# Performance work log

Measured on AMD Instinct MI355X. Metric: run time of the kernel, lower is better.

## Reference

```python
import jax, jax.numpy as jnp
import numpy as np

DIM = 1024
NUM_HEADS = 16
HEAD_DIM = DIM // NUM_HEADS


def setup_inputs() -> dict:
    key = jax.random.key(0)
    k1, k2, k3, k4, k5 = jax.random.split(key, 5)
    s = 0.02
    return {
        "x": jax.random.normal(k1, (2, 2048, DIM), dtype=jnp.float32),
        "Wq": jax.random.normal(k2, (DIM, DIM), dtype=jnp.float32) * s,
        "Wk": jax.random.normal(k3, (DIM, DIM), dtype=jnp.float32) * s,
        "Wv": jax.random.normal(k4, (DIM, DIM), dtype=jnp.float32) * s,
        "Wo": jax.random.normal(k5, (DIM, DIM), dtype=jnp.float32) * s,
    }


def rotate_half(x):
    x1, x2 = x[..., : x.shape[-1] // 2], x[..., x.shape[-1] // 2 :]
    return jnp.concatenate([-x2, x1], axis=-1)


def rope_cos_sin(seq_len, head_dim, dtype):
    inv_freq = 1.0 / (10000.0 ** (jnp.arange(0, head_dim, 2, dtype=jnp.float32) / head_dim))
    t = jnp.arange(seq_len, dtype=jnp.float32)
    freqs = jnp.einsum("i,j->ij", t, inv_freq)  # [S, head_dim/2]
    emb = jnp.concatenate([freqs, freqs], axis=-1)  # [S, head_dim]
    return jnp.cos(emb).astype(dtype), jnp.sin(emb).astype(dtype)


def reference(x, Wq, Wk, Wv, Wo):
    B, S, D = x.shape
    H, Hd = NUM_HEADS, HEAD_DIM
    scale = Hd ** -0.5

    def proj(W):
        # nn.Linear: x @ W.T; reshape to [B, H, S, Hd]
        return (x @ W.T).reshape(B, S, H, Hd).transpose(0, 2, 1, 3)

    q, k, v = proj(Wq), proj(Wk), proj(Wv)
    cos, sin = rope_cos_sin(S, Hd, x.dtype)  # [S, Hd], broadcast over B,H
    q = q * cos + rotate_half(q) * sin
    k = k * cos + rotate_half(k) * sin

    attn = jnp.einsum("bhqd,bhkd->bhqk", q, k) * scale  # [B,H,S,S]
    causal = jnp.triu(jnp.ones((S, S), dtype=bool), k=1)
    attn = jnp.where(causal, -jnp.inf, attn)
    attn = jax.nn.softmax(attn, axis=-1)
    out = jnp.einsum("bhqk,bhkd->bhqd", attn, v)
    out = out.transpose(0, 2, 1, 3).reshape(B, S, D)
    return out @ Wo.T
```

## Files before the change

kernel.cpp:

```cpp
#include <hip/hip_runtime.h>

#define DIM 1024
#define NHEADS 16
#define HD 64
#define SEQ 2048
#define BATCH 2
#define MROWS (BATCH*SEQ)
#define QKVLD 3072

typedef _Float16 h16;
typedef __attribute__((ext_vector_type(2))) _Float16 h16x2;
typedef __attribute__((ext_vector_type(2))) __fp16 fp16x2;
typedef __attribute__((ext_vector_type(4))) _Float16 h16x4;
typedef __attribute__((ext_vector_type(8))) _Float16 h16x8;
typedef __attribute__((ext_vector_type(4))) float f32x4;
typedef __attribute__((ext_vector_type(16))) float f32x16;

union U2 { fp16x2 g; h16x2 h; unsigned u; };

#define CBAR() do { asm volatile("" ::: "memory"); __builtin_amdgcn_s_barrier(); \
                    asm volatile("" ::: "memory"); } while (0)

__global__ __launch_bounds__(256) void prep_k(
    const float* __restrict__ x,  const float* __restrict__ wq,
    const float* __restrict__ wk, const float* __restrict__ wv,
    const float* __restrict__ wo,
    h16* __restrict__ xh, h16* __restrict__ wqkvh, h16* __restrict__ woh,
    float2* __restrict__ rope)
{
    const int NX = MROWS * DIM / 4;
    const int NW = DIM * DIM / 4;
    int gid = blockIdx.x * 256 + threadIdx.x;
    if (gid < NX) {
        float4 v = *reinterpret_cast<const float4*>(x + (size_t)gid * 4);
        h16x4 o; o.x=(h16)v.x; o.y=(h16)v.y; o.z=(h16)v.z; o.w=(h16)v.w;
        *reinterpret_cast<h16x4*>(xh + (size_t)gid * 4) = o;
    } else if (gid < NX + 3 * NW) {
        int j = gid - NX;
        int w = j >> 18, e = j & (NW - 1);
        const float* s = (w == 0) ? wq : (w == 1) ? wk : wv;
        float4 v = *reinterpret_cast<const float4*>(s + (size_t)e * 4);
        h16x4 o; o.x=(h16)v.x; o.y=(h16)v.y; o.z=(h16)v.z; o.w=(h16)v.w;
        *reinterpret_cast<h16x4*>(wqkvh + (size_t)w * DIM * DIM + (size_t)e * 4) = o;
    } else if (gid < NX + 4 * NW) {
        int e = gid - NX - 3 * NW;
        float4 v = *reinterpret_cast<const float4*>(wo + (size_t)e * 4);
        h16x4 o; o.x=(h16)v.x; o.y=(h16)v.y; o.z=(h16)v.z; o.w=(h16)v.w;
        *reinterpret_cast<h16x4*>(woh + (size_t)e * 4) = o;
    } else {
        int t = gid - NX - 4 * NW;
        int s = t >> 5, j = t & 31;
        float inv = powf(10000.0f, -(float)j / 32.0f);
        float ang = (float)s * inv;
        rope[t] = make_float2(cosf(ang), sinf(ang));
    }
}

__global__ __launch_bounds__(512, 2) void gemm256_qkv(
    const h16* __restrict__ A, const h16* __restrict__ Bw,
    h16* __restrict__ C, const float2* __restrict__ rope)
{
    __shared__ h16 As[2][256][64];
    __shared__ h16 Bs[2][256][64];
    const int tid = threadIdx.x, wave = tid >> 6, lane = tid & 63;
    const int lr = lane & 15, lg = lane >> 4;
    const int wm = wave >> 2, wn = wave & 3;
    const int xr = blockIdx.x & 7, jr = blockIdx.x >> 3;
    const int bm = ((xr >> 1) << 2) + (jr & 3);
    const int bn = (xr & 1) * 6 + (jr >> 2);
    const int m0 = bm << 8, n0 = bn << 8;

    const int srl = lane >> 3;
    const int sgc = ((lane & 7) ^ srl) << 3;

#define STAGE_HALF(buf, k0_, h_) do {                                               \
    _Pragma("unroll")                                                               \
    for (int j_ = 0; j_ < 2; ++j_) {                                                \
        int rl_ = ((h_) & 1) * 128 + (j_ * 8 + wave) * 8;                           \
        if ((h_) < 2) {                                                             \
            const h16* g_ = A + (size_t)(m0 + rl_ + srl) * DIM + (k0_) + sgc;       \
            __builtin_amdgcn_global_load_lds(                                       \
                (const __attribute__((address_space(1))) void*)g_,                  \
                (__attribute__((address_space(3))) void*)(&As[buf][rl_][0]), 16, 0, 0); \
        } else {                                                                    \
            const h16* g_ = Bw + (size_t)(n0 + rl_ + srl) * DIM + (k0_) + sgc;      \
            __builtin_amdgcn_global_load_lds(                                       \
                (const __attribute__((address_space(1))) void*)g_,                  \
                (__attribute__((address_space(3))) void*)(&Bs[buf][rl_][0]), 16, 0, 0); \
        }                                                                           \
    }                                                                               \
} while (0)

    f32x4 acc[8][4];
#pragma unroll
    for (int i = 0; i < 8; ++i)
#pragma unroll
        for (int j = 0; j < 4; ++j) acc[i][j] = (f32x4){0.f, 0.f, 0.f, 0.f};

    const int NT = DIM >> 6;
#pragma unroll
    for (int h = 0; h < 4; ++h) STAGE_HALF(0, 0, h);

    int cur = 0;
    for (int t = 0; t < NT; ++t) {
        const int k0n = (t + 1) << 6;
        const bool pf = (t + 1 < NT);
        h16x8 bfr[4][2];
#pragma unroll
        for (int p = 0; p < 4; ++p) {
            if (pf) STAGE_HALF(cur ^ 1, k0n, p);
            if (p == 0) {
                if (pf) asm volatile("s_waitcnt vmcnt(2)" ::: "memory");
                else    asm volatile("s_waitcnt vmcnt(0)" ::: "memory");
                CBAR();
            }
            h16x8 afr[2][2];
#pragma unroll
            for (int e = 0; e < 2; ++e)
#pragma unroll
                for (int ks = 0; ks < 2; ++ks) {
                    int r = wm * 128 + (2 * p + e) * 16 + lr;
                    int cpos = ((ks << 2) + lg) ^ (lr & 7);
                    afr[e][ks] = *(const h16x8*)&As[cur][r][cpos << 3];
                }
            if (p == 0) {
#pragma unroll
                for (int ni = 0; ni < 4; ++ni)
#pragma unroll
                    for (int ks = 0; ks < 2; ++ks) {
                        int r = wn * 64 + ni * 16 + lr;
                        int cpos = ((ks << 2) + lg) ^ (lr & 7);
                        bfr[ni][ks] = *(const h16x8*)&Bs[cur][r][cpos << 3];
                    }
            } else {
                CBAR();
            }
            __builtin_amdgcn_s_setprio(1);
#pragma unroll
            for (int e = 0; e < 2; ++e)
#pragma unroll
                for (int ni = 0; ni < 4; ++ni)
#pragma unroll
                    for (int ks = 0; ks < 2; ++ks)
                        acc[2 * p + e][ni] = __builtin_amdgcn_mfma_f32_16x16x32_f16(
                            afr[e][ks], bfr[ni][ks], acc[2 * p + e][ni], 0, 0, 0);
            __builtin_amdgcn_s_setprio(0);
            CBAR();
        }
        cur ^= 1;
    }
#undef STAGE_HALF

    const int region = n0 >> 10;
    if (region == 2) {
#pragma unroll
        for (int mi = 0; mi < 8; ++mi)
#pragma unroll
            for (int i = 0; i < 4; ++i) {
                int row = m0 + wm * 128 + mi * 16 + lg * 4 + i;
#pragma unroll
                for (int ni = 0; ni < 4; ++ni) {
                    int col = n0 + wn * 64 + ni * 16 + lr;
                    C[(size_t)row * QKVLD + col] = (h16)acc[mi][ni][i];
                }
            }
    } else {
#pragma unroll
        for (int mi = 0; mi < 8; ++mi)
#pragma unroll
            for (int i = 0; i < 4; ++i) {
                int row = m0 + wm * 128 + mi * 16 + lg * 4 + i;
                int s = row & (SEQ - 1);
#pragma unroll
                for (int ni = 0; ni < 4; ++ni) {
                    int col = n0 + wn * 64 + ni * 16 + lr;
                    int d = col & 63;
                    float2 cs = rope[(s << 5) + (d & 31)];
                    float v  = acc[mi][ni][i];
                    float vp = acc[mi][ni ^ 2][i];
                    float rh = (d < 32) ? -vp : vp;
                    C[(size_t)row * QKVLD + col] = (h16)(v * cs.x + rh * cs.y);
                }
            }
    }
}

__global__ __launch_bounds__(256) void gemm_out(
    const h16* __restrict__ A, const h16* __restrict__ Bw,
    float* __restrict__ C, int M, int N, int K)
{
    __shared__ h16 As[2][128][64];
    __shared__ h16 Bs[2][128][64];
    const int tid  = threadIdx.x;
    const int wave = tid >> 6, lane = tid & 63;
    const int lr = lane & 15, lg = lane >> 4;
    const int wm = wave >> 1, wn = wave & 1;
    const int xr = blockIdx.x & 7, jr = blockIdx.x >> 3;
    const int bm = ((xr >> 1) << 3) + (jr & 7);
    const int bn = ((xr & 1) << 2) + (jr >> 3);
    const int m0 = bm << 7, n0 = bn << 7;

    f32x4 acc[4][4];
#pragma unroll
    for (int i = 0; i < 4; ++i)
#pragma unroll
        for (int j = 0; j < 4; ++j) acc[i][j] = (f32x4){0.f, 0.f, 0.f, 0.f};

    const int arow = lane >> 3;
    const int acol = (lane & 7) << 3;

#define GSTAGE(buf, k0_) do {                                                      \
    _Pragma("unroll")                                                              \
    for (int q_ = 0; q_ < 4; ++q_) {                                               \
        int ch_ = wave * 4 + q_;                                                   \
        const h16* ga_ = A + (size_t)(m0 + ch_ * 8 + arow) * K + (k0_) + acol;     \
        __builtin_amdgcn_global_load_lds(                                          \
            (const __attribute__((address_space(1))) void*)ga_,                    \
            (__attribute__((address_space(3))) void*)(&As[buf][ch_ * 8][0]), 16, 0, 0); \
        const h16* gb_ = Bw + (size_t)(n0 + ch_ * 8 + arow) * K + (k0_) + acol;    \
        __builtin_amdgcn_global_load_lds(                                          \
            (const __attribute__((address_space(1))) void*)gb_,                    \
            (__attribute__((address_space(3))) void*)(&Bs[buf][ch_ * 8][0]), 16, 0, 0); \
    }                                                                              \
} while (0)

    const int NT = K >> 6;
    GSTAGE(0, 0);
    __syncthreads();
    int cur = 0;
    for (int t = 0; t < NT; ++t) {
        if (t + 1 < NT) GSTAGE(cur ^ 1, (t + 1) << 6);
#pragma unroll
        for (int ks = 0; ks < 2; ++ks) {
            h16x8 af[4], bf[4];
#pragma unroll
            for (int mi = 0; mi < 4; ++mi)
                af[mi] = *(const h16x8*)&As[cur][wm * 64 + mi * 16 + lr][ks * 32 + lg * 8];
#pragma unroll
            for (int ni = 0; ni < 4; ++ni)
                bf[ni] = *(const h16x8*)&Bs[cur][wn * 64 + ni * 16 + lr][ks * 32 + lg * 8];
#pragma unroll
            for (int mi = 0; mi < 4; ++mi)
#pragma unroll
                for (int ni = 0; ni < 4; ++ni)
                    acc[mi][ni] = __builtin_amdgcn_mfma_f32_16x16x32_f16(
                        af[mi], bf[ni], acc[mi][ni], 0, 0, 0);
        }
        __syncthreads();
        cur ^= 1;
    }
#undef GSTAGE

#pragma unroll
    for (int mi = 0; mi < 4; ++mi)
#pragma unroll
        for (int i = 0; i < 4; ++i) {
            int row = m0 + wm * 64 + mi * 16 + lg * 4 + i;
#pragma unroll
            for (int ni = 0; ni < 4; ++ni) {
                int col = n0 + wn * 64 + ni * 16 + lr;
                C[(size_t)row * N + col] = acc[mi][ni][i];
            }
        }
}

__global__ __launch_bounds__(512) void attn_k(
    const h16* __restrict__ QKV, h16* __restrict__ O)
{
    __shared__ h16 Ks[2][64][64];
    __shared__ h16 Vt[2][64][72];

    const int bx = blockIdx.x, by = blockIdx.y;
    const int b = by >> 4, h = by & 15;
    const int tid = threadIdx.x, wave = tid >> 6, lane = tid & 63;
    const int lq = lane & 31, hi = lane >> 5;
    const int qlo = bx, qhi = 15 - bx;

    const h16* Qb = QKV + (size_t)b * SEQ * QKVLD + h * HD;
    const h16* Kb = Qb + DIM;
    const h16* Vb = Qb + 2 * DIM;

    const int qw0 = (wave < 4) ? (qlo * 128 + wave * 32)
                               : (qhi * 128 + (wave - 4) * 32);

    h16x8 qf[4];
    {
        const h16* qp = Qb + (size_t)(qw0 + lq) * QKVLD + 8 * hi;
        const h16 qs = (h16)(0.125f * 1.44269504f);
#pragma unroll
        for (int kb = 0; kb < 4; ++kb) {
            qf[kb] = *(const h16x8*)(qp + 16 * kb);
            qf[kb] *= qs;
        }
    }

    float l_run = 0.f;
    f32x16 accd[2];
#pragma unroll
    for (int i = 0; i < 16; ++i) { accd[0][i] = 0.f; accd[1][i] = 0.f; }

    const int kwave = wave - 4;
    const int kr = (tid & 255) >> 3, kc = tid & 7;
    h16x8 vv0, vv1;

#define STAGE_K(bufi, kv0_) do {                                                   \
    const h16* gk0_ = Kb + (size_t)((kv0_) + kr) * QKVLD + ((kc ^ (kr & 7)) << 3); \
    __builtin_amdgcn_global_load_lds(                                              \
        (const __attribute__((address_space(1))) void*)gk0_,                       \
        (__attribute__((address_space(3))) void*)(&Ks[bufi][kwave * 8][0]), 16, 0, 0); \
    const h16* gk1_ = Kb + (size_t)((kv0_) + 32 + kr) * QKVLD + ((kc ^ (kr & 7)) << 3); \
    __builtin_amdgcn_global_load_lds(                                              \
        (const __attribute__((address_space(1))) void*)gk1_,                       \
        (__attribute__((address_space(3))) void*)(&Ks[bufi][32 + kwave * 8][0]), 16, 0, 0); \
} while (0)

#define VLOAD(kv0_) do {                                                           \
    const h16* gv_ = Vb + (size_t)((kv0_) + lane) * QKVLD + 16 * wave;             \
    vv0 = *(const h16x8*)gv_; vv1 = *(const h16x8*)(gv_ + 8);                      \
} while (0)

#define VWRITE(bufi) do {                                                          \
    _Pragma("unroll")                                                              \
    for (int j_ = 0; j_ < 8; ++j_) {                                               \
        Vt[bufi][16 * wave + j_][lane] = vv0[j_];                                  \
        Vt[bufi][16 * wave + 8 + j_][lane] = vv1[j_];                              \
    }                                                                              \
} while (0)

    const int nkv = 2 * qhi + 2;
    if (wave >= 4) STAGE_K(0, 0);
    else { VLOAD(0); VWRITE(0); }
    __syncthreads();

    for (int t = 0; t < nkv; ++t) {
        const int cur = t & 1;
        const int kv0 = t << 6;
        const bool pf = (t + 1 < nkv);
        if (pf) {
            if (wave >= 4) STAGE_K(cur ^ 1, kv0 + 64);
            else VLOAD(kv0 + 64);
        }

        const bool act = (kv0 <= qw0 + 31);
        float p[32];
        if (act) {
            f32x16 s0, s1;
#pragma unroll
            for (int i = 0; i < 16; ++i) { s0[i] = 0.f; s1[i] = 0.f; }
            const int sk = lq & 7;
            __builtin_amdgcn_s_setprio(1);
#pragma unroll
            for (int kb = 0; kb < 4; ++kb) {
                const int ch = ((2 * kb + hi) ^ sk) << 3;
                h16x8 kf0 = *(const h16x8*)&Ks[cur][lq][ch];
                h16x8 kf1 = *(const h16x8*)&Ks[cur][32 + lq][ch];
                s0 = __builtin_amdgcn_mfma_f32_32x32x16_f16(kf0, qf[kb], s0, 0, 0, 0);
                s1 = __builtin_amdgcn_mfma_f32_32x32x16_f16(kf1, qf[kb], s1, 0, 0, 0);
            }
            __builtin_amdgcn_s_setprio(0);
            const bool full = (kv0 + 64 <= qw0);
            float ls = 0.f;
            if (full) {
#pragma unroll
                for (int r = 0; r < 16; ++r) {
                    p[r]      = exp2f(s0[r]);
                    p[16 + r] = exp2f(s1[r]);
                    ls += p[r] + p[16 + r];
                }
            } else {
                const int Lq = qw0 + lq - kv0;
#pragma unroll
                for (int r = 0; r < 16; ++r) {
                    const int kvl = (r & 3) + 8 * (r >> 2) + 4 * hi;
                    float e0 = exp2f(s0[r]);
                    float e1 = exp2f(s1[r]);
                    p[r]      = (kvl <= Lq)      ? e0 : 0.f;
                    p[16 + r] = (kvl + 32 <= Lq) ? e1 : 0.f;
                    ls += p[r] + p[16 + r];
                }
            }
            l_run += ls;
        }
        if (pf && wave < 4) VWRITE(cur ^ 1);
        if (act) {
            h16x8 pfrag[4];
#pragma unroll
            for (int kva = 0; kva < 2; ++kva) {
                const int o = 16 * kva;
                U2 x, y, z, w, x2, y2, z2, w2;
                x.g  = __builtin_amdgcn_cvt_pkrtz(p[o+0],  p[o+1]);
                y.g  = __builtin_amdgcn_cvt_pkrtz(p[o+2],  p[o+3]);
                z.g  = __builtin_amdgcn_cvt_pkrtz(p[o+4],  p[o+5]);
                w.g  = __builtin_amdgcn_cvt_pkrtz(p[o+6],  p[o+7]);
                x2.g = __builtin_amdgcn_cvt_pkrtz(p[o+8],  p[o+9]);
                y2.g = __builtin_amdgcn_cvt_pkrtz(p[o+10], p[o+11]);
                z2.g = __builtin_amdgcn_cvt_pkrtz(p[o+12], p[o+13]);
                w2.g = __builtin_amdgcn_cvt_pkrtz(p[o+14], p[o+15]);
                asm volatile("v_permlane32_swap_b32 %0, %1" : "+v"(x.u),  "+v"(z.u));
                asm volatile("v_permlane32_swap_b32 %0, %1" : "+v"(y.u),  "+v"(w.u));
                asm volatile("v_permlane32_swap_b32 %0, %1" : "+v"(x2.u), "+v"(z2.u));
                asm volatile("v_permlane32_swap_b32 %0, %1" : "+v"(y2.u), "+v"(w2.u));
                h16x8 f0, f1;
                f0[0]=x.h.x;  f0[1]=x.h.y;  f0[2]=y.h.x;  f0[3]=y.h.y;
                f0[4]=z.h.x;  f0[5]=z.h.y;  f0[6]=w.h.x;  f0[7]=w.h.y;
                f1[0]=x2.h.x; f1[1]=x2.h.y; f1[2]=y2.h.x; f1[3]=y2.h.y;
                f1[4]=z2.h.x; f1[5]=z2.h.y; f1[6]=w2.h.x; f1[7]=w2.h.y;
                pfrag[2*kva]   = f0;
                pfrag[2*kva+1] = f1;
            }
            __builtin_amdgcn_s_setprio(1);
#pragma unroll
            for (int da = 0; da < 2; ++da)
#pragma unroll
                for (int kvb = 0; kvb < 4; ++kvb) {
                    h16x8 vf = *(const h16x8*)&Vt[cur][32 * da + lq][16 * kvb + 8 * hi];
                    accd[da] = __builtin_amdgcn_mfma_f32_32x32x16_f16(vf, pfrag[kvb], accd[da], 0, 0, 0);
                }
            __builtin_amdgcn_s_setprio(0);
        }
        __syncthreads();
    }

    float lt = l_run + __shfl_xor(l_run, 32);
    float inv = 1.0f / lt;
    h16* Ob = O + (size_t)b * SEQ * DIM + h * HD + (size_t)(qw0 + lq) * DIM;
#pragma unroll
    for (int da = 0; da < 2; ++da)
#pragma unroll
        for (int r = 0; r < 16; r += 2) {
            int d = 32 * da + (r & 3) + 8 * (r >> 2) + 4 * hi;
            h16x2 ov;
            ov.x = (h16)(accd[da][r] * inv);
            ov.y = (h16)(accd[da][r + 1] * inv);
            *(h16x2*)(Ob + d) = ov;
        }
#undef STAGE_K
#undef VLOAD
#undef VWRITE
}

extern "C" void kernel_launch(void* const* d_in, const int* in_sizes, int n_in,
                              void* d_out, int out_size, void* d_ws, size_t ws_size,
                              hipStream_t stream)
{
    const float* x  = (const float*)d_in[0];
    const float* Wq = (const float*)d_in[1];
    const float* Wk = (const float*)d_in[2];
    const float* Wv = (const float*)d_in[3];
    const float* Wo = (const float*)d_in[4];

    char* ws = (char*)d_ws;
    h16* xh     = (h16*)(ws);
    h16* wqkvh  = (h16*)(ws + ((size_t)8  << 20));
    h16* woh    = (h16*)(ws + ((size_t)14 << 20));
    h16* QKVd   = (h16*)(ws + ((size_t)16 << 20));
    h16* Od     = (h16*)(ws + ((size_t)40 << 20));
    float2* rope = (float2*)(ws + ((size_t)48 << 20));

    const int NX = MROWS * DIM / 4, NW = DIM * DIM / 4;
    prep_k<<<(NX + 4 * NW + SEQ * 32) / 256, 256, 0, stream>>>(
        x, Wq, Wk, Wv, Wo, xh, wqkvh, woh, rope);

    gemm256_qkv<<<(MROWS / 256) * (QKVLD / 256), 512, 0, stream>>>(
        xh, wqkvh, QKVd, rope);

    attn_k<<<dim3(8, BATCH * NHEADS), 512, 0, stream>>>(QKVd, Od);

    gemm_out<<<(MROWS / 128) * (DIM / 128), 256, 0, stream>>>(
        Od, woh, (float*)d_out, MROWS, DIM, DIM);
}
```

Measured before the change: 140.7 us.

## Double KV tile per barrier to 128 and skip masked upper S-block MFMAs

The attention loop now stages 128 KV rows per iteration, processed as two 64-row sub-tiles, which halves the number of barriers and prefetch rounds per block. It also skips the second 32-row QK^T MFMA group when it lies entirely above the causal diagonal. The cost is doubled LDS use for the K and V buffers, which may reduce occupancy, and more registers for the extra V prefetch. The last partial tile may also load K/V rows that are never needed.

```diff
diff --git a/kernel.cpp b/kernel.cpp
--- a/kernel.cpp
+++ b/kernel.cpp
@@ -267,8 +267,8 @@
 __global__ __launch_bounds__(512) void attn_k(
     const h16* __restrict__ QKV, h16* __restrict__ O)
 {
-    __shared__ h16 Ks[2][64][64];
-    __shared__ h16 Vt[2][64][72];
+    __shared__ h16 Ks[2][128][64];
+    __shared__ h16 Vt[2][64][136];
 
     const int bx = blockIdx.x, by = blockIdx.y;
     const int b = by >> 4, h = by & 15;
@@ -301,122 +301,136 @@
 
     const int kwave = wave - 4;
     const int kr = (tid & 255) >> 3, kc = tid & 7;
-    h16x8 vv0, vv1;
+    h16x8 vv0, vv1, vv2, vv3;
 
 #define STAGE_K(bufi, kv0_) do {                                                   \
-    const h16* gk0_ = Kb + (size_t)((kv0_) + kr) * QKVLD + ((kc ^ (kr & 7)) << 3); \
-    __builtin_amdgcn_global_load_lds(                                              \
-        (const __attribute__((address_space(1))) void*)gk0_,                       \
-        (__attribute__((address_space(3))) void*)(&Ks[bufi][kwave * 8][0]), 16, 0, 0); \
-    const h16* gk1_ = Kb + (size_t)((kv0_) + 32 + kr) * QKVLD + ((kc ^ (kr & 7)) << 3); \
-    __builtin_amdgcn_global_load_lds(                                              \
-        (const __attribute__((address_space(1))) void*)gk1_,                       \
-        (__attribute__((address_space(3))) void*)(&Ks[bufi][32 + kwave * 8][0]), 16, 0, 0); \
+    _Pragma("unroll")                                                              \
+    for (int j_ = 0; j_ < 4; ++j_) {                                               \
+        const h16* gk_ = Kb + (size_t)((kv0_) + 32 * j_ + kr) * QKVLD              \
+                            + ((kc ^ (kr & 7)) << 3);                              \
+        __builtin_amdgcn_global_load_lds(                                          \
+            (const __attribute__((address_space(1))) void*)gk_,                    \
+            (__attribute__((address_space(3))) void*)(&Ks[bufi][32 * j_ + kwave * 8][0]), \
+            16, 0, 0);                                                             \
+    }                                                                              \
 } while (0)
 
 #define VLOAD(kv0_) do {                                                           \
     const h16* gv_ = Vb + (size_t)((kv0_) + lane) * QKVLD + 16 * wave;             \
     vv0 = *(const h16x8*)gv_; vv1 = *(const h16x8*)(gv_ + 8);                      \
+    const h16* gw_ = Vb + (size_t)((kv0_) + 64 + lane) * QKVLD + 16 * wave;        \
+    vv2 = *(const h16x8*)gw_; vv3 = *(const h16x8*)(gw_ + 8);                      \
 } while (0)
 
 #define VWRITE(bufi) do {                                                          \
     _Pragma("unroll")                                                              \
     for (int j_ = 0; j_ < 8; ++j_) {                                               \
-        Vt[bufi][16 * wave + j_][lane] = vv0[j_];                                  \
-        Vt[bufi][16 * wave + 8 + j_][lane] = vv1[j_];                              \
+        Vt[bufi][16 * wave + j_][lane]          = vv0[j_];                         \
+        Vt[bufi][16 * wave + 8 + j_][lane]      = vv1[j_];                         \
+        Vt[bufi][16 * wave + j_][64 + lane]     = vv2[j_];                         \
+        Vt[bufi][16 * wave + 8 + j_][64 + lane] = vv3[j_];                         \
     }                                                                              \
 } while (0)
 
-    const int nkv = 2 * qhi + 2;
+    const int nkv = qhi + 1;
     if (wave >= 4) STAGE_K(0, 0);
     else { VLOAD(0); VWRITE(0); }
     __syncthreads();
 
     for (int t = 0; t < nkv; ++t) {
         const int cur = t & 1;
-        const int kv0 = t << 6;
+        const int kv0t = t << 7;
         const bool pf = (t + 1 < nkv);
         if (pf) {
-            if (wave >= 4) STAGE_K(cur ^ 1, kv0 + 64);
-            else VLOAD(kv0 + 64);
-        }
-
-        const bool act = (kv0 <= qw0 + 31);
-        float p[32];
-        if (act) {
-            f32x16 s0, s1;
-#pragma unroll
-            for (int i = 0; i < 16; ++i) { s0[i] = 0.f; s1[i] = 0.f; }
-            const int sk = lq & 7;
-            __builtin_amdgcn_s_setprio(1);
-#pragma unroll
-            for (int kb = 0; kb < 4; ++kb) {
-                const int ch = ((2 * kb + hi) ^ sk) << 3;
-                h16x8 kf0 = *(const h16x8*)&Ks[cur][lq][ch];
-                h16x8 kf1 = *(const h16x8*)&Ks[cur][32 + lq][ch];
-                s0 = __builtin_amdgcn_mfma_f32_32x32x16_f16(kf0, qf[kb], s0, 0, 0, 0);
-                s1 = __builtin_amdgcn_mfma_f32_32x32x16_f16(kf1, qf[kb], s1, 0, 0, 0);
-            }
-            __builtin_amdgcn_s_setprio(0);
-            const bool full = (kv0 + 64 <= qw0);
-            float ls = 0.f;
-            if (full) {
-#pragma unroll
-                for (int r = 0; r < 16; ++r) {
-                    p[r]      = exp2f(s0[r]);
-                    p[16 + r] = exp2f(s1[r]);
-                    ls += p[r] + p[16 + r];
-                }
-            } else {
-                const int Lq = qw0 + lq - kv0;
-#pragma unroll
-                for (int r = 0; r < 16; ++r) {
-                    const int kvl = (r & 3) + 8 * (r >> 2) + 4 * hi;
-                    float e0 = exp2f(s0[r]);
-                    float e1 = exp2f(s1[r]);
-                    p[r]      = (kvl <= Lq)      ? e0 : 0.f;
-                    p[16 + r] = (kvl + 32 <= Lq) ? e1 : 0.f;
-                    ls += p[r] + p[16 + r];
-                }
-            }
-            l_run += ls;
-        }
-        if (pf && wave < 4) VWRITE(cur ^ 1);
-        if (act) {
-            h16x8 pfrag[4];
-#pragma unroll
-            for (int kva = 0; kva < 2; ++kva) {
-                const int o = 16 * kva;
-                U2 x, y, z, w, x2, y2, z2, w2;
-                x.g  = __builtin_amdgcn_cvt_pkrtz(p[o+0],  p[o+1]);
-                y.g  = __builtin_amdgcn_cvt_pkrtz(p[o+2],  p[o+3]);
-                z.g  = __builtin_amdgcn_cvt_pkrtz(p[o+4],  p[o+5]);
-                w.g  = __builtin_amdgcn_cvt_pkrtz(p[o+6],  p[o+7]);
-                x2.g = __builtin_amdgcn_cvt_pkrtz(p[o+8],  p[o+9]);
-                y2.g = __builtin_amdgcn_cvt_pkrtz(p[o+10], p[o+11]);
-                z2.g = __builtin_amdgcn_cvt_pkrtz(p[o+12], p[o+13]);
-                w2.g = __builtin_amdgcn_cvt_pkrtz(p[o+14], p[o+15]);
-                asm volatile("v_permlane32_swap_b32 %0, %1" : "+v"(x.u),  "+v"(z.u));
-                asm volatile("v_permlane32_swap_b32 %0, %1" : "+v"(y.u),  "+v"(w.u));
-                asm volatile("v_permlane32_swap_b32 %0, %1" : "+v"(x2.u), "+v"(z2.u));
-                asm volatile("v_permlane32_swap_b32 %0, %1" : "+v"(y2.u), "+v"(w2.u));
-                h16x8 f0, f1;
-                f0[0]=x.h.x;  f0[1]=x.h.y;  f0[2]=y.h.x;  f0[3]=y.h.y;
-                f0[4]=z.h.x;  f0[5]=z.h.y;  f0[6]=w.h.x;  f0[7]=w.h.y;
-                f1[0]=x2.h.x; f1[1]=x2.h.y; f1[2]=y2.h.x; f1[3]=y2.h.y;
-                f1[4]=z2.h.x; f1[5]=z2.h.y; f1[6]=w2.h.x; f1[7]=w2.h.y;
-                pfrag[2*kva]   = f0;
-                pfrag[2*kva+1] = f1;
-            }
-            __builtin_amdgcn_s_setprio(1);
-#pragma unroll
-            for (int da = 0; da < 2; ++da)
-#pragma unroll
-                for (int kvb = 0; kvb < 4; ++kvb) {
-                    h16x8 vf = *(const h16x8*)&Vt[cur][32 * da + lq][16 * kvb + 8 * hi];
-                    accd[da] = __builtin_amdgcn_mfma_f32_32x32x16_f16(vf, pfrag[kvb], accd[da], 0, 0, 0);
-                }
-            __builtin_amdgcn_s_setprio(0);
+            if (wave >= 4) STAGE_K(cur ^ 1, kv0t + 128);
+            else VLOAD(kv0t + 128);
+        }
+
+#pragma unroll
+        for (int g = 0; g < 2; ++g) {
+            const int kv0 = kv0t + (g << 6);
+            const bool act = (kv0 <= qw0 + 31);
+            if (act) {
+                f32x16 s0, s1;
+#pragma unroll
+                for (int i = 0; i < 16; ++i) { s0[i] = 0.f; s1[i] = 0.f; }
+                const int sk = lq & 7;
+                const bool upper = (kv0 + 32 <= qw0 + 31);
+                __builtin_amdgcn_s_setprio(1);
+#pragma unroll
+                for (int kb = 0; kb < 4; ++kb) {
+                    const int ch = ((2 * kb + hi) ^ sk) << 3;
+                    h16x8 kf0 = *(const h16x8*)&Ks[cur][(g << 6) + lq][ch];
+                    s0 = __builtin_amdgcn_mfma_f32_32x32x16_f16(kf0, qf[kb], s0, 0, 0, 0);
+                }
+                if (upper) {
+#pragma unroll
+                    for (int kb = 0; kb < 4; ++kb) {
+                        const int ch = ((2 * kb + hi) ^ sk) << 3;
+                        h16x8 kf1 = *(const h16x8*)&Ks[cur][(g << 6) + 32 + lq][ch];
+                        s1 = __builtin_amdgcn_mfma_f32_32x32x16_f16(kf1, qf[kb], s1, 0, 0, 0);
+                    }
+                }
+                __builtin_amdgcn_s_setprio(0);
+                const bool full = (kv0 + 64 <= qw0);
+                float p[32];
+                float ls = 0.f;
+                if (full) {
+#pragma unroll
+                    for (int r = 0; r < 16; ++r) {
+                        p[r]      = exp2f(s0[r]);
+                        p[16 + r] = exp2f(s1[r]);
+                        ls += p[r] + p[16 + r];
+                    }
+                } else {
+                    const int Lq = qw0 + lq - kv0;
+#pragma unroll
+                    for (int r = 0; r < 16; ++r) {
+                        const int kvl = (r & 3) + 8 * (r >> 2) + 4 * hi;
+                        float e0 = exp2f(s0[r]);
+                        float e1 = upper ? exp2f(s1[r]) : 0.f;
+                        p[r]      = (kvl <= Lq)      ? e0 : 0.f;
+                        p[16 + r] = (kvl + 32 <= Lq) ? e1 : 0.f;
+                        ls += p[r] + p[16 + r];
+                    }
+                }
+                l_run += ls;
+                h16x8 pfrag[4];
+#pragma unroll
+                for (int kva = 0; kva < 2; ++kva) {
+                    const int o = 16 * kva;
+                    U2 x, y, z, w, x2, y2, z2, w2;
+                    x.g  = __builtin_amdgcn_cvt_pkrtz(p[o+0],  p[o+1]);
+                    y.g  = __builtin_amdgcn_cvt_pkrtz(p[o+2],  p[o+3]);
+                    z.g  = __builtin_amdgcn_cvt_pkrtz(p[o+4],  p[o+5]);
+                    w.g  = __builtin_amdgcn_cvt_pkrtz(p[o+6],  p[o+7]);
+                    x2.g = __builtin_amdgcn_cvt_pkrtz(p[o+8],  p[o+9]);
+                    y2.g = __builtin_amdgcn_cvt_pkrtz(p[o+10], p[o+11]);
+                    z2.g = __builtin_amdgcn_cvt_pkrtz(p[o+12], p[o+13]);
+                    w2.g = __builtin_amdgcn_cvt_pkrtz(p[o+14], p[o+15]);
+                    asm volatile("v_permlane32_swap_b32 %0, %1" : "+v"(x.u),  "+v"(z.u));
+                    asm volatile("v_permlane32_swap_b32 %0, %1" : "+v"(y.u),  "+v"(w.u));
+                    asm volatile("v_permlane32_swap_b32 %0, %1" : "+v"(x2.u), "+v"(z2.u));
+                    asm volatile("v_permlane32_swap_b32 %0, %1" : "+v"(y2.u), "+v"(w2.u));
+                    h16x8 f0, f1;
+                    f0[0]=x.h.x;  f0[1]=x.h.y;  f0[2]=y.h.x;  f0[3]=y.h.y;
+                    f0[4]=z.h.x;  f0[5]=z.h.y;  f0[6]=w.h.x;  f0[7]=w.h.y;
+                    f1[0]=x2.h.x; f1[1]=x2.h.y; f1[2]=y2.h.x; f1[3]=y2.h.y;
+                    f1[4]=z2.h.x; f1[5]=z2.h.y; f1[6]=w2.h.x; f1[7]=w2.h.y;
+                    pfrag[2*kva]   = f0;
+                    pfrag[2*kva+1] = f1;
+                }
+                __builtin_amdgcn_s_setprio(1);
+#pragma unroll
+                for (int da = 0; da < 2; ++da)
+#pragma unroll
+                    for (int kvb = 0; kvb < 4; ++kvb) {
+                        h16x8 vf = *(const h16x8*)&Vt[cur][32 * da + lq][(g << 6) + 16 * kvb + 8 * hi];
+                        accd[da] = __builtin_amdgcn_mfma_f32_32x32x16_f16(vf, pfrag[kvb], accd[da], 0, 0, 0);
+                    }
+                __builtin_amdgcn_s_setprio(0);
+            }
+            if (g == 0 && pf && wave < 4) VWRITE(cur ^ 1);
         }
         __syncthreads();
     }
```

New measurement: 143.2 us. No clear change (+1.8%).
